# Kernel tuning notes

Measured on AMD Instinct MI355X. Metric: run time of the kernel, lower is better.

The kernel has to match this reference:

```python
import jax, jax.numpy as jnp
import numpy as np

D_MODEL = 1024
NUM_HEADS = 16
D_HEAD = D_MODEL // NUM_HEADS
D_FF = 4096
B, T = 2, 2048
THETA = 10000.0
EPS = 1e-5


def setup_inputs() -> dict:
    key = jax.random.key(0)
    ks = jax.random.split(key, 6)
    def tn(k, shape, fan_in, fan_out):
        std = np.sqrt(2.0 / (fan_in + fan_out))
        return jax.random.normal(k, shape, dtype=jnp.float32) * std
    return {
        "x": jax.random.normal(ks[0], (B, T, D_MODEL), dtype=jnp.float32),
        "W_qkv": tn(ks[1], (3 * D_MODEL, D_MODEL), D_MODEL, 3 * D_MODEL),
        "W_o": tn(ks[2], (D_MODEL, D_MODEL), D_MODEL, D_MODEL),
        "g1": jnp.ones((D_MODEL,), dtype=jnp.float32),
        "g2": jnp.ones((D_MODEL,), dtype=jnp.float32),
        "W1": tn(ks[3], (D_FF, D_MODEL), D_MODEL, D_FF),
        "W2": tn(ks[4], (D_MODEL, D_FF), D_FF, D_MODEL),
        "W3": tn(ks[5], (D_FF, D_MODEL), D_MODEL, D_FF),
    }


def _rmsnorm(x, g):
    xf = x.astype(jnp.float32)
    rms = jnp.sqrt(jnp.mean(xf * xf, axis=-1, keepdims=True) + EPS)
    return (xf / rms * g).astype(x.dtype)


def _rope(t, cos, sin):
    # t: [B,H,T,dh]; interleaved (even,odd) pairs treated as complex numbers
    tr = t.reshape(*t.shape[:-1], D_HEAD // 2, 2)
    te, to = tr[..., 0], tr[..., 1]
    out = jnp.stack([te * cos - to * sin, te * sin + to * cos], axis=-1)
    return out.reshape(t.shape)


def reference(x, W_qkv, W_o, g1, g2, W1, W2, W3):
    Bx, Tx, C = x.shape
    # --- attention sub-block (pre-norm) ---
    h = _rmsnorm(x, g1)
    qkv = jnp.einsum('btc,jc->btj', h, W_qkv)                # [B,T,3C]
    qkv = qkv.reshape(Bx, Tx, 3, NUM_HEADS, D_HEAD)
    qkv = jnp.transpose(qkv, (2, 0, 3, 1, 4))                # [3,B,H,T,dh]
    q, k, v = qkv[0], qkv[1], qkv[2]
    # RoPE tables for positions arange(T)
    inv = 1.0 / (THETA ** (jnp.arange(0, D_HEAD, 2, dtype=jnp.float32) / D_HEAD))
    ang = jnp.arange(Tx, dtype=jnp.float32)[:, None] * inv[None, :]   # [T,dh/2]
    cos, sin = jnp.cos(ang), jnp.sin(ang)                    # broadcast over B,H
    q = _rope(q, cos, sin)
    k = _rope(k, cos, sin)
    scores = jnp.einsum('bhqd,bhkd->bhqk', q, k) / jnp.sqrt(jnp.float32(D_HEAD))
    causal = jnp.tril(jnp.ones((Tx, Tx), dtype=bool))
    scores = jnp.where(causal, scores, -jnp.inf)
    probs = jax.nn.softmax(scores, axis=-1)
    attn = jnp.einsum('bhqk,bhkd->bhqd', probs, v)           # [B,H,T,dh]
    attn = jnp.transpose(attn, (0, 2, 1, 3)).reshape(Bx, Tx, C)
    x = x + jnp.einsum('btc,jc->btj', attn, W_o)
    # --- SwiGLU FFN sub-block (pre-norm) ---
    h2 = _rmsnorm(x, g2)
    a = jnp.einsum('btc,fc->btf', h2, W1)
    b = jnp.einsum('btc,fc->btf', h2, W3)
    ffn = jnp.einsum('btf,cf->btc', (a * jax.nn.sigmoid(a)) * b, W2)
    return x + ffn
```

## Files before the change

### kernel.cpp

```cpp
#include <hip/hip_runtime.h>
#include <math.h>

typedef __bf16 bf16_t;
typedef __bf16 bf16x2 __attribute__((ext_vector_type(2)));
typedef __bf16 bf16x4 __attribute__((ext_vector_type(4)));
typedef __bf16 bf16x8 __attribute__((ext_vector_type(8)));
typedef float  f32x4  __attribute__((ext_vector_type(4)));

#define D_MODEL 1024
#define T_SEQ   2048
#define BATCH   2
#define NHEAD   16
#define DHEAD   64
#define DFF     4096
#define ROWS    (BATCH * T_SEQ)

static __device__ __forceinline__ void gload_lds16(const void* g, void* l) {
  __builtin_amdgcn_global_load_lds((const __attribute__((address_space(1))) void*)g,
                                   (__attribute__((address_space(3))) void*)l,
                                   16, 0, 0);
}

__global__ __launch_bounds__(256) void cvt_bf16_kernel(const float* __restrict__ in,
                                                       bf16_t* __restrict__ out, int n) {
  int i = (blockIdx.x * 256 + threadIdx.x) * 4;
  if (i >= n) return;
  float4 v = *(const float4*)(in + i);
  bf16x4 o;
  o[0] = (bf16_t)v.x; o[1] = (bf16_t)v.y; o[2] = (bf16_t)v.z; o[3] = (bf16_t)v.w;
  *(bf16x4*)(out + i) = o;
}

__global__ __launch_bounds__(256) void rope_tables_kernel(float* __restrict__ cost,
                                                          float* __restrict__ sint) {
  int i = blockIdx.x * 256 + threadIdx.x;
  int t = i >> 5, p = i & 31;
  double inv = pow(10000.0, -(double)(2 * p) / 64.0);
  double ang = (double)t * inv;
  cost[i] = (float)cos(ang);
  sint[i] = (float)sin(ang);
}

__global__ __launch_bounds__(256) void rmsnorm_kernel(const float* __restrict__ x,
                                                      const float* __restrict__ g,
                                                      bf16_t* __restrict__ out) {
  const int row = blockIdx.x;
  const int tid = threadIdx.x;
  const float4 v = ((const float4*)(x + (size_t)row * D_MODEL))[tid];
  float ss = v.x * v.x + v.y * v.y + v.z * v.z + v.w * v.w;
#pragma unroll
  for (int m = 32; m >= 1; m >>= 1) ss += __shfl_xor(ss, m);
  __shared__ float red[4];
  if ((tid & 63) == 0) red[tid >> 6] = ss;
  __syncthreads();
  float tot = red[0] + red[1] + red[2] + red[3];
  const float rinv = 1.0f / sqrtf(tot * (1.0f / D_MODEL) + 1e-5f);
  const float4 gv = ((const float4*)g)[tid];
  bf16x4 o;
  o[0] = (bf16_t)(v.x * rinv * gv.x);
  o[1] = (bf16_t)(v.y * rinv * gv.y);
  o[2] = (bf16_t)(v.z * rinv * gv.z);
  o[3] = (bf16_t)(v.w * rinv * gv.w);
  *(bf16x4*)(out + (size_t)row * D_MODEL + tid * 4) = o;
}

__global__ __launch_bounds__(256) void rope_scatter_kernel(const bf16_t* __restrict__ qkv,
                                                           const float* __restrict__ cost,
                                                           const float* __restrict__ sint,
                                                           bf16_t* __restrict__ Q,
                                                           bf16_t* __restrict__ K) {
  int i = blockIdx.x * 256 + threadIdx.x;
  int p = i & 31;
  int h = (i >> 5) & 15;
  int t = (i >> 9) & 2047;
  int b = i >> 20;
  const bf16_t* base = qkv + (size_t)(b * T_SEQ + t) * (3 * D_MODEL) + h * DHEAD + 2 * p;
  float qe = (float)base[0],            qo = (float)base[1];
  float ke = (float)base[D_MODEL],      ko = (float)base[D_MODEL + 1];
  float c = cost[t * 32 + p], s = sint[t * 32 + p];
  size_t o = ((size_t)(b * NHEAD + h) * T_SEQ + t) * DHEAD + 2 * p;
  bf16x2 qv, kv;
  qv[0] = (bf16_t)(qe * c - qo * s); qv[1] = (bf16_t)(qe * s + qo * c);
  kv[0] = (bf16_t)(ke * c - ko * s); kv[1] = (bf16_t)(ke * s + ko * c);
  *(bf16x2*)(Q + o) = qv;
  *(bf16x2*)(K + o) = kv;
}

__global__ __launch_bounds__(256) void vt_kernel(const bf16_t* __restrict__ qkv,
                                                 bf16_t* __restrict__ Vt) {
  __shared__ bf16_t ld[64 * 72];
  const int tid = threadIdx.x;
  const int tt = blockIdx.x;
  const int bh = blockIdx.y;
  const int b = bh >> 4, h = bh & 15;
#pragma unroll
  for (int it = 0; it < 2; ++it) {
    int idx = it * 256 + tid;
    int r = idx >> 3, cc = (idx & 7) * 8;
    bf16x8 v = *(const bf16x8*)&qkv[(size_t)(b * T_SEQ + tt * 64 + r) * (3 * D_MODEL)
                                    + 2 * D_MODEL + h * DHEAD + cc];
    *(bf16x8*)&ld[r * 72 + cc] = v;
  }
  __syncthreads();
#pragma unroll
  for (int it = 0; it < 2; ++it) {
    int idx = it * 256 + tid;
    int d = idx >> 3, t8 = (idx & 7) * 8;
    bf16x8 v;
#pragma unroll
    for (int j = 0; j < 8; ++j) v[j] = ld[(t8 + j) * 72 + d];
    *(bf16x8*)&Vt[(((size_t)bh * 32 + tt) * 64 + d) * 64 + t8] = v;
  }
}

template <int EPI, int BM, int BN>
__global__ __launch_bounds__(256) void gemm_bt(const bf16_t* __restrict__ A,
                                               const bf16_t* __restrict__ B,
                                               void* __restrict__ Cout,
                                               const float* __restrict__ res,
                                               int M, int N, int K, int gxn) {
  constexpr int MR = BM / 32, NR = BN / 32;
  __shared__ __align__(16) bf16_t lA[BM * 64];
  __shared__ __align__(16) bf16_t lB[BN * 64];
  const int tid = threadIdx.x;
  const int wave = tid >> 6, lane = tid & 63;
  const int lr = lane & 15, lg = lane >> 4;
  const int nwg = gridDim.x;
  const int bid = blockIdx.x;
  const int swz = (bid & 7) * (nwg >> 3) + (bid >> 3);
  const int bx = swz % gxn, by = swz / gxn;
  const int brow = by * BM, bcol = bx * BN;
  const int wr = (wave >> 1) * (BM / 2), wc = (wave & 1) * (BN / 2);
  f32x4 acc[MR][NR] = {};
  for (int k0 = 0; k0 < K; k0 += 64) {
    __syncthreads();
#pragma unroll
    for (int r = 0; r < BM / 32; ++r) {
      const int base = r * 4096 + wave * 1024;
      const int fb = base + lane * 16;
      const int row = fb >> 7;
      const int e = (fb & 127) >> 1;
      gload_lds16(A + (size_t)(brow + row) * K + k0 + e, (char*)lA + base);
    }
#pragma unroll
    for (int r = 0; r < BN / 32; ++r) {
      const int base = r * 4096 + wave * 1024;
      const int fb = base + lane * 16;
      const int row = fb >> 7;
      const int e = (fb & 127) >> 1;
      gload_lds16(B + (size_t)(bcol + row) * K + k0 + e, (char*)lB + base);
    }
    __syncthreads();
    bf16x8 aF[MR][2], bF[NR][2];
#pragma unroll
    for (int mi = 0; mi < MR; ++mi)
#pragma unroll
      for (int h = 0; h < 2; ++h)
        aF[mi][h] = *(const bf16x8*)&lA[(wr + mi * 16 + lr) * 64 + h * 32 + 8 * lg];
#pragma unroll
    for (int ni = 0; ni < NR; ++ni)
#pragma unroll
      for (int h = 0; h < 2; ++h)
        bF[ni][h] = *(const bf16x8*)&lB[(wc + ni * 16 + lr) * 64 + h * 32 + 8 * lg];
#pragma unroll
    for (int h = 0; h < 2; ++h)
#pragma unroll
      for (int mi = 0; mi < MR; ++mi)
#pragma unroll
        for (int ni = 0; ni < NR; ++ni)
          acc[mi][ni] = __builtin_amdgcn_mfma_f32_16x16x32_bf16(aF[mi][h], bF[ni][h], acc[mi][ni], 0, 0, 0);
  }
  const int rb = brow + wr + lg * 4;
  const int cb = bcol + wc + lr;
  if (EPI == 0) {
    bf16_t* C = (bf16_t*)Cout;
#pragma unroll
    for (int mi = 0; mi < MR; ++mi)
#pragma unroll
      for (int ni = 0; ni < NR; ++ni)
#pragma unroll
        for (int i = 0; i < 4; ++i)
          C[(size_t)(rb + mi * 16 + i) * N + cb + ni * 16] = (bf16_t)acc[mi][ni][i];
  } else {
    float* C = (float*)Cout;
#pragma unroll
    for (int mi = 0; mi < MR; ++mi)
#pragma unroll
      for (int ni = 0; ni < NR; ++ni)
#pragma unroll
        for (int i = 0; i < 4; ++i) {
          size_t idx = (size_t)(rb + mi * 16 + i) * N + cb + ni * 16;
          C[idx] = acc[mi][ni][i] + res[idx];
        }
  }
}

__global__ __launch_bounds__(256, 4) void attn_kernel(const bf16_t* __restrict__ Q,
                                                      const bf16_t* __restrict__ K,
                                                      const bf16_t* __restrict__ Vt,
                                                      bf16_t* __restrict__ attn) {
  __shared__ __align__(16) bf16_t kbuf[2][64 * 64];
  __shared__ __align__(16) bf16_t vbuf[2][64 * 64];
  __shared__ __align__(16) bf16_t pbuf[4][16 * 64];
  const int tid = threadIdx.x;
  const int wave = tid >> 6, lane = tid & 63;
  const int lr = lane & 15, lg = lane >> 4;
  const int bid = blockIdx.x;
  const int x = bid & 7, u = bid >> 3;
  const int bh = x * 4 + (u & 3);
  const int v = u >> 2;
  const int tile = (7 * v + 5 * (u & 3) + x) & 31;
  const int b = bh >> 4, hh = bh & 15;
  const size_t hb = (size_t)bh * T_SEQ * DHEAD;
  const bf16_t* Qb = Q + hb;
  const bf16_t* Kb = K + hb;
  const bf16_t* Vb = Vt + hb;
  char* pwc = (char*)pbuf[wave];
  const int q0 = tile * 64 + wave * 16;
  const int c0 = wave * 2, c1 = wave * 2 + 1;
  const int so = (lane * 16) ^ ((lane >> 3) << 4);

  bf16x8 qf[2];
#pragma unroll
  for (int h = 0; h < 2; ++h)
    qf[h] = *(const bf16x8*)&Qb[(size_t)(q0 + lr) * DHEAD + h * 32 + 8 * lg];
  f32x4 o[4] = {};
  float mrun = -INFINITY, lsum = 0.0f;
  const int nit = tile + 1;

  {
    const char* kg = (const char*)Kb;
    const char* vg = (const char*)Vb;
    gload_lds16(kg + c0 * 1024 + so, (char*)kbuf[0] + c0 * 1024);
    gload_lds16(kg + c1 * 1024 + so, (char*)kbuf[0] + c1 * 1024);
    gload_lds16(vg + c0 * 1024 + so, (char*)vbuf[0] + c0 * 1024);
    gload_lds16(vg + c1 * 1024 + so, (char*)vbuf[0] + c1 * 1024);
  }
  __syncthreads();
  int cur = 0;

  for (int it = 0; it < nit; ++it) {
    const int k0 = it * 64;
    if (it + 1 < nit) {
      const char* kg = (const char*)(Kb + (size_t)(k0 + 64) * DHEAD);
      const char* vg = (const char*)(Vb + (size_t)(it + 1) * 4096);
      char* kd = (char*)kbuf[cur ^ 1];
      char* vd = (char*)vbuf[cur ^ 1];
      gload_lds16(kg + c0 * 1024 + so, kd + c0 * 1024);
      gload_lds16(kg + c1 * 1024 + so, kd + c1 * 1024);
      gload_lds16(vg + c0 * 1024 + so, vd + c0 * 1024);
      gload_lds16(vg + c1 * 1024 + so, vd + c1 * 1024);
    }
    const char* kl = (const char*)kbuf[cur];
    const char* vl = (const char*)vbuf[cur];
    f32x4 s[4] = {};
#pragma unroll
    for (int c = 0; c < 4; ++c) {
      const int tr = c * 16 + lr;
      const int sw = (tr & 7) << 4;
      bf16x8 kf0 = *(const bf16x8*)(kl + tr * 128 + ((16 * lg) ^ sw));
      bf16x8 kf1 = *(const bf16x8*)(kl + tr * 128 + ((64 + 16 * lg) ^ sw));
      s[c] = __builtin_amdgcn_mfma_f32_16x16x32_bf16(kf0, qf[0], s[c], 0, 0, 0);
      s[c] = __builtin_amdgcn_mfma_f32_16x16x32_bf16(kf1, qf[1], s[c], 0, 0, 0);
    }
    const bool dm = (k0 + 63 > q0);
#pragma unroll
    for (int c = 0; c < 4; ++c)
#pragma unroll
      for (int i = 0; i < 4; ++i) {
        float sv = s[c][i] * 0.125f;
        if (dm && (k0 + c * 16 + lg * 4 + i > q0 + lr)) sv = -INFINITY;
        s[c][i] = sv;
      }
    float bm = s[0][0];
#pragma unroll
    for (int c = 0; c < 4; ++c)
#pragma unroll
      for (int i = 0; i < 4; ++i) bm = fmaxf(bm, s[c][i]);
    bm = fmaxf(bm, __shfl_xor(bm, 16));
    bm = fmaxf(bm, __shfl_xor(bm, 32));
    if (!__all(bm <= mrun)) {
      const float mn = fmaxf(mrun, bm);
      const float al = __expf(mrun - mn);
      mrun = mn;
      lsum *= al;
#pragma unroll
      for (int dd = 0; dd < 4; ++dd)
#pragma unroll
        for (int i = 0; i < 4; ++i) o[dd][i] *= al;
    }
    float bs = 0.0f;
#pragma unroll
    for (int c = 0; c < 4; ++c)
#pragma unroll
      for (int i = 0; i < 4; ++i) {
        float e = __expf(s[c][i] - mrun);
        s[c][i] = e;
        bs += e;
      }
    bs += __shfl_xor(bs, 16);
    bs += __shfl_xor(bs, 32);
    lsum += bs;
#pragma unroll
    for (int c = 0; c < 4; ++c) {
      bf16x4 pb;
#pragma unroll
      for (int i = 0; i < 4; ++i) pb[i] = (bf16_t)s[c][i];
      const int byt = (lr * 128 + ((c * 32 + lg * 8) ^ ((lr & 7) << 4)));
      *(bf16x4*)(pwc + byt) = pb;
    }
    asm volatile("s_waitcnt lgkmcnt(0)" ::: "memory");
    __builtin_amdgcn_sched_barrier(0);
    bf16x8 pT[2];
#pragma unroll
    for (int h = 0; h < 2; ++h)
      pT[h] = *(const bf16x8*)(pwc + (lr * 128 + ((h * 64 + 16 * lg) ^ ((lr & 7) << 4))));
#pragma unroll
    for (int dd = 0; dd < 4; ++dd) {
      const int vr = dd * 16 + lr;
      const int sw = (vr & 7) << 4;
      bf16x8 vf0 = *(const bf16x8*)(vl + vr * 128 + ((16 * lg) ^ sw));
      bf16x8 vf1 = *(const bf16x8*)(vl + vr * 128 + ((64 + 16 * lg) ^ sw));
      o[dd] = __builtin_amdgcn_mfma_f32_16x16x32_bf16(vf0, pT[0], o[dd], 0, 0, 0);
      o[dd] = __builtin_amdgcn_mfma_f32_16x16x32_bf16(vf1, pT[1], o[dd], 0, 0, 0);
    }
    __syncthreads();
    cur ^= 1;
  }
  const float rls = 1.0f / lsum;
  bf16_t* orow = attn + (size_t)(b * T_SEQ + q0 + lr) * D_MODEL + hh * DHEAD;
#pragma unroll
  for (int dd = 0; dd < 4; ++dd) {
    bf16x4 ov;
#pragma unroll
    for (int i = 0; i < 4; ++i) ov[i] = (bf16_t)(o[dd][i] * rls);
    *(bf16x4*)(orow + dd * 16 + lg * 4) = ov;
  }
}

__global__ __launch_bounds__(256) void swiglu_kernel(bf16_t* __restrict__ a,
                                                     const bf16_t* __restrict__ b) {
  size_t i = ((size_t)blockIdx.x * 256 + threadIdx.x) * 8;
  bf16x8 va = *(const bf16x8*)(a + i);
  bf16x8 vb = *(const bf16x8*)(b + i);
  bf16x8 og;
#pragma unroll
  for (int j = 0; j < 8; ++j) {
    float av = (float)va[j];
    float bv = (float)vb[j];
    float gv = av / (1.0f + __expf(-av)) * bv;
    og[j] = (bf16_t)gv;
  }
  *(bf16x8*)(a + i) = og;
}

extern "C" void kernel_launch(void* const* d_in, const int* in_sizes, int n_in,
                              void* d_out, int out_size, void* d_ws, size_t ws_size,
                              hipStream_t stream) {
  const float* x    = (const float*)d_in[0];
  const float* Wqkv = (const float*)d_in[1];
  const float* Wo   = (const float*)d_in[2];
  const float* g1   = (const float*)d_in[3];
  const float* g2   = (const float*)d_in[4];
  const float* W1   = (const float*)d_in[5];
  const float* W2   = (const float*)d_in[6];
  const float* W3   = (const float*)d_in[7];
  float* out = (float*)d_out;
  char* ws = (char*)d_ws;
  const size_t MB = 1024 * 1024;

  float*  x1   = (float*)(ws + 0);
  bf16_t* h    = (bf16_t*)(ws + 16 * MB);
  bf16_t* attn = (bf16_t*)(ws + 16 * MB);
  bf16_t* h2   = (bf16_t*)(ws + 16 * MB);
  bf16_t* qkv  = (bf16_t*)(ws + 24 * MB);
  bf16_t* Qb   = (bf16_t*)(ws + 48 * MB);
  bf16_t* Kb   = (bf16_t*)(ws + 56 * MB);
  bf16_t* Vt   = (bf16_t*)(ws + 64 * MB);
  bf16_t* abuf = (bf16_t*)(ws + 24 * MB);
  bf16_t* bbuf = (bf16_t*)(ws + 56 * MB);
  float*  cost = (float*)(ws + 88 * MB);
  float*  sint = (float*)(ws + 88 * MB + 262144);
  bf16_t* wq_b = (bf16_t*)(ws + 89 * MB);
  bf16_t* wo_b = (bf16_t*)(ws + 95 * MB);
  bf16_t* w1_b = (bf16_t*)(ws + 97 * MB);
  bf16_t* w3_b = (bf16_t*)(ws + 105 * MB);
  bf16_t* w2_b = (bf16_t*)(ws + 113 * MB);

  cvt_bf16_kernel<<<3 * D_MODEL * D_MODEL / 1024, 256, 0, stream>>>(Wqkv, wq_b, 3 * D_MODEL * D_MODEL);
  cvt_bf16_kernel<<<D_MODEL * D_MODEL / 1024, 256, 0, stream>>>(Wo, wo_b, D_MODEL * D_MODEL);
  cvt_bf16_kernel<<<DFF * D_MODEL / 1024, 256, 0, stream>>>(W1, w1_b, DFF * D_MODEL);
  cvt_bf16_kernel<<<DFF * D_MODEL / 1024, 256, 0, stream>>>(W3, w3_b, DFF * D_MODEL);
  cvt_bf16_kernel<<<DFF * D_MODEL / 1024, 256, 0, stream>>>(W2, w2_b, DFF * D_MODEL);
  rope_tables_kernel<<<(T_SEQ * 32) / 256, 256, 0, stream>>>(cost, sint);

  rmsnorm_kernel<<<ROWS, 256, 0, stream>>>(x, g1, h);
  gemm_bt<0, 128, 128><<<768, 256, 0, stream>>>(h, wq_b, qkv, nullptr,
                                                ROWS, 3 * D_MODEL, D_MODEL, 24);
  rope_scatter_kernel<<<(BATCH * T_SEQ * NHEAD * 32) / 256, 256, 0, stream>>>(
      qkv, cost, sint, Qb, Kb);
  vt_kernel<<<dim3(T_SEQ / 64, BATCH * NHEAD), 256, 0, stream>>>(qkv, Vt);
  attn_kernel<<<1024, 256, 0, stream>>>(Qb, Kb, Vt, attn);
  gemm_bt<1, 64, 64><<<1024, 256, 0, stream>>>(attn, wo_b, x1, x,
                                               ROWS, D_MODEL, D_MODEL, 16);

  rmsnorm_kernel<<<ROWS, 256, 0, stream>>>(x1, g2, h2);
  gemm_bt<0, 128, 128><<<1024, 256, 0, stream>>>(h2, w1_b, abuf, nullptr,
                                                 ROWS, DFF, D_MODEL, 32);
  gemm_bt<0, 128, 128><<<1024, 256, 0, stream>>>(h2, w3_b, bbuf, nullptr,
                                                 ROWS, DFF, D_MODEL, 32);
  swiglu_kernel<<<(ROWS * DFF) / (256 * 8), 256, 0, stream>>>(abuf, bbuf);
  gemm_bt<1, 64, 64><<<1024, 256, 0, stream>>>(abuf, w2_b, out, x1,
                                               ROWS, D_MODEL, DFF, 16);
}
```

Baseline: 494.7 us.

## Fuse W1/W3 GEMMs, merge weight conversions, enlarge output-projection tiles

Result: faster. 473.7 us (-4.2%).

```diff
diff --git a/kernel.cpp b/kernel.cpp
--- a/kernel.cpp
+++ b/kernel.cpp
@@ -21,14 +21,26 @@
                                    16, 0, 0);
 }
 
-__global__ __launch_bounds__(256) void cvt_bf16_kernel(const float* __restrict__ in,
-                                                       bf16_t* __restrict__ out, int n) {
-  int i = (blockIdx.x * 256 + threadIdx.x) * 4;
-  if (i >= n) return;
-  float4 v = *(const float4*)(in + i);
+__global__ __launch_bounds__(256) void cvt_all_kernel(const float* __restrict__ Wqkv,
+                                                      const float* __restrict__ Wo,
+                                                      const float* __restrict__ W1,
+                                                      const float* __restrict__ W3,
+                                                      const float* __restrict__ W2,
+                                                      bf16_t* __restrict__ wq,
+                                                      bf16_t* __restrict__ wo,
+                                                      bf16_t* __restrict__ w13,
+                                                      bf16_t* __restrict__ w2) {
+  int i = blockIdx.x * 256 + threadIdx.x;
+  const float* src; bf16_t* dst; int off;
+  if (i < 786432)       { src = Wqkv; dst = wq;            off = i; }
+  else if (i < 1048576) { src = Wo;   dst = wo;            off = i - 786432; }
+  else if (i < 2097152) { src = W1;   dst = w13;           off = i - 1048576; }
+  else if (i < 3145728) { src = W3;   dst = w13 + 4194304; off = i - 2097152; }
+  else                  { src = W2;   dst = w2;            off = i - 3145728; }
+  float4 v = ((const float4*)src)[off];
   bf16x4 o;
   o[0] = (bf16_t)v.x; o[1] = (bf16_t)v.y; o[2] = (bf16_t)v.z; o[3] = (bf16_t)v.w;
-  *(bf16x4*)(out + i) = o;
+  *(bf16x4*)(dst + off * 4) = o;
 }
 
 __global__ __launch_bounds__(256) void rope_tables_kernel(float* __restrict__ cost,
@@ -118,7 +130,7 @@
                                                const bf16_t* __restrict__ B,
                                                void* __restrict__ Cout,
                                                const float* __restrict__ res,
-                                               int M, int N, int K, int gxn) {
+                                               int M, int N, int K, int lda, int gxn) {
   constexpr int MR = BM / 32, NR = BN / 32;
   __shared__ __align__(16) bf16_t lA[BM * 64];
   __shared__ __align__(16) bf16_t lB[BN * 64];
@@ -140,7 +152,7 @@
       const int fb = base + lane * 16;
       const int row = fb >> 7;
       const int e = (fb & 127) >> 1;
-      gload_lds16(A + (size_t)(brow + row) * K + k0 + e, (char*)lA + base);
+      gload_lds16(A + (size_t)(brow + row) * lda + k0 + e, (char*)lA + base);
     }
 #pragma unroll
     for (int r = 0; r < BN / 32; ++r) {
@@ -338,11 +350,13 @@
   }
 }
 
-__global__ __launch_bounds__(256) void swiglu_kernel(bf16_t* __restrict__ a,
-                                                     const bf16_t* __restrict__ b) {
-  size_t i = ((size_t)blockIdx.x * 256 + threadIdx.x) * 8;
-  bf16x8 va = *(const bf16x8*)(a + i);
-  bf16x8 vb = *(const bf16x8*)(b + i);
+__global__ __launch_bounds__(256) void swiglu_kernel(bf16_t* __restrict__ a13) {
+  int i = blockIdx.x * 256 + threadIdx.x;
+  int r = i >> 9;
+  int c = (i & 511) * 8;
+  bf16_t* pa = a13 + (size_t)r * 8192 + c;
+  bf16x8 va = *(const bf16x8*)pa;
+  bf16x8 vb = *(const bf16x8*)(pa + 4096);
   bf16x8 og;
 #pragma unroll
   for (int j = 0; j < 8; ++j) {
@@ -351,7 +365,7 @@
     float gv = av / (1.0f + __expf(-av)) * bv;
     og[j] = (bf16_t)gv;
   }
-  *(bf16x8*)(a + i) = og;
+  *(bf16x8*)pa = og;
 }
 
 extern "C" void kernel_launch(void* const* d_in, const int* in_sizes, int n_in,
@@ -369,47 +383,39 @@
   char* ws = (char*)d_ws;
   const size_t MB = 1024 * 1024;
 
-  float*  x1   = (float*)(ws + 0);
-  bf16_t* h    = (bf16_t*)(ws + 16 * MB);
-  bf16_t* attn = (bf16_t*)(ws + 16 * MB);
-  bf16_t* h2   = (bf16_t*)(ws + 16 * MB);
-  bf16_t* qkv  = (bf16_t*)(ws + 24 * MB);
-  bf16_t* Qb   = (bf16_t*)(ws + 48 * MB);
-  bf16_t* Kb   = (bf16_t*)(ws + 56 * MB);
-  bf16_t* Vt   = (bf16_t*)(ws + 64 * MB);
-  bf16_t* abuf = (bf16_t*)(ws + 24 * MB);
-  bf16_t* bbuf = (bf16_t*)(ws + 56 * MB);
-  float*  cost = (float*)(ws + 88 * MB);
-  float*  sint = (float*)(ws + 88 * MB + 262144);
-  bf16_t* wq_b = (bf16_t*)(ws + 89 * MB);
-  bf16_t* wo_b = (bf16_t*)(ws + 95 * MB);
-  bf16_t* w1_b = (bf16_t*)(ws + 97 * MB);
-  bf16_t* w3_b = (bf16_t*)(ws + 105 * MB);
-  bf16_t* w2_b = (bf16_t*)(ws + 113 * MB);
-
-  cvt_bf16_kernel<<<3 * D_MODEL * D_MODEL / 1024, 256, 0, stream>>>(Wqkv, wq_b, 3 * D_MODEL * D_MODEL);
-  cvt_bf16_kernel<<<D_MODEL * D_MODEL / 1024, 256, 0, stream>>>(Wo, wo_b, D_MODEL * D_MODEL);
-  cvt_bf16_kernel<<<DFF * D_MODEL / 1024, 256, 0, stream>>>(W1, w1_b, DFF * D_MODEL);
-  cvt_bf16_kernel<<<DFF * D_MODEL / 1024, 256, 0, stream>>>(W3, w3_b, DFF * D_MODEL);
-  cvt_bf16_kernel<<<DFF * D_MODEL / 1024, 256, 0, stream>>>(W2, w2_b, DFF * D_MODEL);
+  float*  x1    = (float*)(ws + 0);
+  bf16_t* h     = (bf16_t*)(ws + 16 * MB);
+  bf16_t* attn  = (bf16_t*)(ws + 16 * MB);
+  bf16_t* h2    = (bf16_t*)(ws + 16 * MB);
+  bf16_t* qkv   = (bf16_t*)(ws + 24 * MB);
+  bf16_t* Qb    = (bf16_t*)(ws + 48 * MB);
+  bf16_t* Kb    = (bf16_t*)(ws + 56 * MB);
+  bf16_t* Vt    = (bf16_t*)(ws + 64 * MB);
+  bf16_t* ab13  = (bf16_t*)(ws + 24 * MB);
+  bf16_t* wq_b  = (bf16_t*)(ws + 88 * MB);
+  bf16_t* wo_b  = (bf16_t*)(ws + 94 * MB);
+  bf16_t* w13_b = (bf16_t*)(ws + 96 * MB);
+  bf16_t* w2_b  = (bf16_t*)(ws + 112 * MB);
+  float*  cost  = (float*)(ws + 120 * MB);
+  float*  sint  = (float*)(ws + 120 * MB + 262144);
+
+  cvt_all_kernel<<<16384, 256, 0, stream>>>(Wqkv, Wo, W1, W3, W2, wq_b, wo_b, w13_b, w2_b);
   rope_tables_kernel<<<(T_SEQ * 32) / 256, 256, 0, stream>>>(cost, sint);
 
   rmsnorm_kernel<<<ROWS, 256, 0, stream>>>(x, g1, h);
   gemm_bt<0, 128, 128><<<768, 256, 0, stream>>>(h, wq_b, qkv, nullptr,
-                                                ROWS, 3 * D_MODEL, D_MODEL, 24);
+                                                ROWS, 3 * D_MODEL, D_MODEL, D_MODEL, 24);
   rope_scatter_kernel<<<(BATCH * T_SEQ * NHEAD * 32) / 256, 256, 0, stream>>>(
       qkv, cost, sint, Qb, Kb);
   vt_kernel<<<dim3(T_SEQ / 64, BATCH * NHEAD), 256, 0, stream>>>(qkv, Vt);
   attn_kernel<<<1024, 256, 0, stream>>>(Qb, Kb, Vt, attn);
-  gemm_bt<1, 64, 64><<<1024, 256, 0, stream>>>(attn, wo_b, x1, x,
-                                               ROWS, D_MODEL, D_MODEL, 16);
+  gemm_bt<1, 128, 64><<<512, 256, 0, stream>>>(attn, wo_b, x1, x,
+                                               ROWS, D_MODEL, D_MODEL, D_MODEL, 16);
 
   rmsnorm_kernel<<<ROWS, 256, 0, stream>>>(x1, g2, h2);
-  gemm_bt<0, 128, 128><<<1024, 256, 0, stream>>>(h2, w1_b, abuf, nullptr,
-                                                 ROWS, DFF, D_MODEL, 32);
-  gemm_bt<0, 128, 128><<<1024, 256, 0, stream>>>(h2, w3_b, bbuf, nullptr,
-                                                 ROWS, DFF, D_MODEL, 32);
-  swiglu_kernel<<<(ROWS * DFF) / (256 * 8), 256, 0, stream>>>(abuf, bbuf);
-  gemm_bt<1, 64, 64><<<1024, 256, 0, stream>>>(abuf, w2_b, out, x1,
-                                               ROWS, D_MODEL, DFF, 16);
-}
+  gemm_bt<0, 128, 128><<<2048, 256, 0, stream>>>(h2, w13_b, ab13, nullptr,
+                                                 ROWS, 2 * DFF, D_MODEL, D_MODEL, 64);
+  swiglu_kernel<<<(ROWS * DFF) / (256 * 8), 256, 0, stream>>>(ab13);
+  gemm_bt<1, 128, 64><<<512, 256, 0, stream>>>(ab13, w2_b, out, x1,
+                                               ROWS, D_MODEL, DFF, 2 * DFF, 16);
+}
```
